# Optimization experiments

Hardware: AMD Instinct MI355X
Metric: run time of the kernel (lower is better)

## Reference

```python
import jax, jax.numpy as jnp
import numpy as np

N, E = 100000, 1600000
H, F, G = 128, 128, 51   # hidden_channels, num_filters, num_gaussians
CUTOFF = 10.0
LOG2 = 0.6931471805599453

def ssp(x):
    # ShiftedSoftplus: softplus(x) - log(2)
    return jax.nn.softplus(x) - jnp.asarray(LOG2, x.dtype)

def setup_inputs() -> dict:
    key = jax.random.key(0)
    ks = jax.random.split(key, 16)
    s = 0.05
    return {
        "z": jax.random.normal(ks[0], (N, H), dtype=jnp.float32),
        "pos": jax.random.uniform(ks[1], (N, 3), dtype=jnp.float32),
        "edge_index": jax.random.randint(ks[2], (2, E), 0, N, dtype=jnp.int64),
        # CFConv linears
        "lin1_w": jax.random.normal(ks[3], (F, H), dtype=jnp.float32) * s,   # no bias
        "lin2_w": jax.random.normal(ks[4], (H, F), dtype=jnp.float32) * s,
        "lin2_b": jnp.zeros((H,), dtype=jnp.float32),
        # edge-filter MLP: Linear(G,F) -> ssp -> Linear(F,F)
        "mlp0_w": jax.random.normal(ks[5], (F, G), dtype=jnp.float32) * s,
        "mlp0_b": jnp.zeros((F,), dtype=jnp.float32),
        "mlp2_w": jax.random.normal(ks[6], (F, F), dtype=jnp.float32) * s,
        "mlp2_b": jnp.zeros((F,), dtype=jnp.float32),
        # InteractionBlock output linear
        "blk_w": jax.random.normal(ks[7], (H, H), dtype=jnp.float32) * s,
        "blk_b": jnp.zeros((H,), dtype=jnp.float32),
        # SchNetLayer head: lin1 -> ssp -> lin2
        "out1_w": jax.random.normal(ks[8], (H, H), dtype=jnp.float32) * s,
        "out1_b": jnp.zeros((H,), dtype=jnp.float32),
        "out2_w": jax.random.normal(ks[9], (H, H), dtype=jnp.float32) * s,
        "out2_b": jnp.zeros((H,), dtype=jnp.float32),
    }

def reference(z, pos, edge_index, lin1_w, lin2_w, lin2_b, mlp0_w, mlp0_b,
              mlp2_w, mlp2_b, blk_w, blk_b, out1_w, out1_b, out2_w, out2_b):
    row, col = edge_index[0], edge_index[1]
    # edge distances
    d = pos[row] - pos[col]                          # [E,3]
    ew = jnp.sqrt(jnp.sum(d * d, axis=-1) + 1e-12)   # [E]
    # GaussianSmearing(0, cutoff, G)
    offset = jnp.linspace(0.0, CUTOFF, G).astype(ew.dtype)
    coeff = -0.5 / (CUTOFF / (G - 1)) ** 2
    ea = jnp.exp(coeff * (ew[:, None] - offset[None, :]) ** 2)  # [E,G]
    # cosine cutoff envelope
    C = 0.5 * (jnp.cos(ew * (jnp.pi / CUTOFF)) + 1.0)           # [E]
    # edge-conditioned filter W = mlp(edge_attr) * C
    W = ssp(ea @ mlp0_w.T + mlp0_b) @ mlp2_w.T + mlp2_b         # [E,F]
    W = W * C[:, None]
    # CFConv: lin1 -> gather(x_j) * W -> scatter-add -> lin2
    x1 = z @ lin1_w.T                                            # [N,F]
    msg = x1[row] * W                                            # [E,F]
    agg = jax.ops.segment_sum(msg, col, num_segments=z.shape[0]) # [N,F]
    conv = agg @ lin2_w.T + lin2_b                               # [N,H]
    # InteractionBlock: act -> lin, residual add
    h = z + (ssp(conv) @ blk_w.T + blk_b)
    # head: lin1 -> ssp -> lin2
    h = ssp(h @ out1_w.T + out1_b) @ out2_w.T + out2_b
    return h
```

## Files before the change

kernel.cpp:

```cpp
#include <hip/hip_runtime.h>
#include <math.h>


#define HDIM 128
#define GDIM 51
#define TAB_T 2048
#define TAB_PTS (TAB_T + 1)
#define RMAX 1.7330f
#define INV_STEP ((float)TAB_T / RMAX)
#define WMAT 2048
#define SCB 2048

typedef short short8 __attribute__((ext_vector_type(8)));
typedef float floatx4 __attribute__((ext_vector_type(4)));

__device__ __forceinline__ float ssp_f(float x) {
  float t = __expf(-fabsf(x));
  return fmaxf(x, 0.0f) + __logf(1.0f + t) - 0.6931471805599453f;
}
__device__ __forceinline__ float bl(unsigned int u) { return __uint_as_float(u << 16); }
__device__ __forceinline__ float bh(unsigned int u) { return __uint_as_float(u & 0xFFFF0000u); }
__device__ __forceinline__ unsigned short f2bf(float f) {
  unsigned int u = __float_as_uint(f);
  unsigned int r = u + 0x7FFFu + ((u >> 16) & 1u);
  return (unsigned short)(r >> 16);
}
__device__ __forceinline__ unsigned int pack_bf16(float a, float b) {
  unsigned int r;
  asm("v_cvt_pk_bf16_f32 %0, %1, %2" : "=v"(r) : "v"(a), "v"(b));
  return r;
}

__global__ void prep_kernel(const float* __restrict__ lin1, const float* __restrict__ lin2,
                            const float* __restrict__ blkw, const float* __restrict__ o1w,
                            const float* __restrict__ o2w, const float* __restrict__ m0w,
                            const float* __restrict__ m2w,
                            unsigned short* __restrict__ wbf,
                            float* __restrict__ m0t, float* __restrict__ m2t) {
  int gid = blockIdx.x * blockDim.x + threadIdx.x;
  int stride = gridDim.x * blockDim.x;
  for (int idx = gid; idx < 5 * 16384; idx += stride) {
    int mat = idx >> 14;
    int o   = idx & 16383;
    int idx4 = o >> 3;
    int jj   = o & 7;
    int ct   = idx4 >> 8;
    int kk   = (idx4 >> 6) & 3;
    int lane = idx4 & 63;
    int c = ct * 16 + (lane & 15);
    int g = kk * 4 + (lane >> 4);
    const float* w = (mat == 0) ? lin1 : (mat == 1) ? lin2 : (mat == 2) ? blkw
                   : (mat == 3) ? o1w : o2w;
    wbf[idx] = f2bf(w[c * HDIM + g * 8 + jj]);
  }
  for (int idx = gid; idx < GDIM * HDIM; idx += stride) {
    int g = idx >> 7, f = idx & 127;
    m0t[idx] = m0w[f * GDIM + g];
  }
  for (int idx = gid; idx < HDIM * HDIM; idx += stride) {
    int j = idx >> 7, f = idx & 127;
    m2t[idx] = m2w[f * HDIM + j];
  }
}

__global__ __launch_bounds__(128) void table_kernel(
    const float* __restrict__ m0t, const float* __restrict__ m0b,
    const float* __restrict__ m2t, const float* __restrict__ m2b,
    unsigned int* __restrict__ tabb) {
  __shared__ float ea[GDIM];
  __shared__ float h1[HDIM];
  int f = threadIdx.x;
  float b0 = m0b[f];
  float b2 = m2b[f];
  for (int t = blockIdx.x; t < TAB_PTS; t += gridDim.x) {
    float ew = (float)t * (RMAX / (float)TAB_T);
    if (f < GDIM) {
      float dd = ew - (float)f * 0.2f;
      ea[f] = expf(-12.5f * dd * dd);
    }
    __syncthreads();
    float s = b0;
    #pragma unroll 3
    for (int g = 0; g < GDIM; ++g) s = fmaf(ea[g], m0t[g * HDIM + f], s);
    h1[f] = ssp_f(s);
    __syncthreads();
    float s2 = b2;
    #pragma unroll 4
    for (int j = 0; j < HDIM; ++j) s2 = fmaf(h1[j], m2t[j * HDIM + f], s2);
    float C = 0.5f * (cosf(ew * 0.31415926535897931f) + 1.0f);
    float val = s2 * C;
    float pr = __shfl_xor(val, 1);
    if ((f & 1) == 0) tabb[(size_t)t * 64 + (f >> 1)] = pack_bf16(val, pr);
    __syncthreads();
  }
}

__device__ __forceinline__ short8 frag_ld(const unsigned int* __restrict__ slab,
                                          int row, int g) {
  const uint4 v = *(const uint4*)(slab + row * 64 + (((g << 2) ^ ((row & 7) << 2))));
  return __builtin_bit_cast(short8, v);
}

__device__ __forceinline__ void stage_act64(unsigned int* __restrict__ slab,
                                            const float* __restrict__ src,
                                            int n0, int N, int t) {
  #pragma unroll
  for (int i = 0; i < 8; ++i) {
    int id = t + i * 256;
    int r  = id >> 5;
    int k4 = id & 31;
    int gn = n0 + r;
    float4 v = make_float4(0.f, 0.f, 0.f, 0.f);
    if (gn < N) v = *(const float4*)(src + (size_t)gn * HDIM + k4 * 4);
    int w = (k4 * 2) ^ ((r & 7) * 4);
    *(uint2*)(slab + r * 64 + w) = make_uint2(pack_bf16(v.x, v.y), pack_bf16(v.z, v.w));
  }
}

__device__ __forceinline__ void stage_mm8(const unsigned int* __restrict__ Aslab,
                                          const uint4* __restrict__ wm,
                                          floatx4 acc[8], int wave, int lane) {
  int m = lane & 15, q = lane >> 4;
  int r0 = wave * 16 + m;
  #pragma unroll
  for (int ct = 0; ct < 8; ++ct) acc[ct] = (floatx4){0.f, 0.f, 0.f, 0.f};
  #pragma unroll
  for (int kk = 0; kk < 4; ++kk) {
    short8 a = frag_ld(Aslab, r0, kk * 4 + q);
    #pragma unroll
    for (int ct = 0; ct < 8; ++ct) {
      short8 b = __builtin_bit_cast(short8, wm[(ct * 4 + kk) * 64 + lane]);
      acc[ct] = __builtin_amdgcn_mfma_f32_16x16x32_bf16(a, b, acc[ct], 0, 0, 0);
    }
  }
}

__device__ __forceinline__ void mm_cs1(const unsigned int* __restrict__ Aslab,
                                       const uint4* __restrict__ wm,
                                       floatx4 acc[4], int ct, int lane) {
  int m = lane & 15, q = lane >> 4;
  #pragma unroll
  for (int mr = 0; mr < 4; ++mr) acc[mr] = (floatx4){0.f, 0.f, 0.f, 0.f};
  #pragma unroll
  for (int kk = 0; kk < 4; ++kk) {
    short8 b = __builtin_bit_cast(short8, wm[(ct * 4 + kk) * 64 + lane]);
    #pragma unroll
    for (int mr = 0; mr < 4; ++mr) {
      short8 a = frag_ld(Aslab, mr * 16 + m, kk * 4 + q);
      acc[mr] = __builtin_amdgcn_mfma_f32_16x16x32_bf16(a, b, acc[mr], 0, 0, 0);
    }
  }
}

__device__ __forceinline__ void wb_cs1(unsigned int* __restrict__ slab,
                                       const floatx4 acc[4], float bias,
                                       int ct, int lane, bool do_ssp) {
  int m = lane & 15, q = lane >> 4;
  bool act = ((m ^ ct) & 1) == 0;
  int k2 = ct * 8 + (m >> 1);
  #pragma unroll
  for (int mr = 0; mr < 4; ++mr) {
    #pragma unroll
    for (int r = 0; r < 4; ++r) {
      float v = acc[mr][r] + bias;
      if (do_ssp) v = ssp_f(v);
      float pr = __shfl_xor(v, 1);
      if (act) {
        int R = mr * 16 + q * 4 + r;
        slab[R * 64 + (k2 ^ ((R & 7) * 4))] = (m & 1) ? pack_bf16(pr, v)
                                                      : pack_bf16(v, pr);
      }
    }
  }
}

__global__ __launch_bounds__(256) void x1_kernel(const float* __restrict__ z,
    const uint4* __restrict__ wbf4, unsigned int* __restrict__ x1b, int N) {
  __shared__ unsigned int Aslab[64 * 64];
  int t = threadIdx.x, wave = t >> 6, lane = t & 63;
  int m = lane & 15, q = lane >> 4;
  int n0 = blockIdx.x * 64;
  stage_act64(Aslab, z, n0, N, t);
  __syncthreads();
  floatx4 acc[8];
  stage_mm8(Aslab, wbf4, acc, wave, lane);
  #pragma unroll
  for (int ct = 0; ct < 8; ++ct) {
    #pragma unroll
    for (int r = 0; r < 4; ++r) {
      float v = acc[ct][r];
      float pr = __shfl_xor(v, 1);
      int gr = n0 + wave * 16 + q * 4 + r;
      if (((m ^ ct) & 1) == 0 && gr < N)
        x1b[(size_t)gr * 64 + ct * 8 + (m >> 1)] = (m & 1) ? pack_bf16(pr, v)
                                                           : pack_bf16(v, pr);
    }
  }
}

__global__ __launch_bounds__(256) void hist_kernel(const int* __restrict__ ei,
                                                   int* __restrict__ count, int E) {
  int gid = blockIdx.x * blockDim.x + threadIdx.x;
  int stride = gridDim.x * blockDim.x;
  for (int e = gid; e < E; e += stride)
    atomicAdd(&count[ei[E + e]], 1);
}

__global__ __launch_bounds__(256) void scan1_kernel(const int* __restrict__ count,
                                                    int* __restrict__ bsum, int N) {
  int b = blockIdx.x, t = threadIdx.x;
  int base = b * SCB;
  int s = 0;
  for (int i = t; i < SCB; i += 256) {
    int gi = base + i;
    s += (gi < N) ? count[gi] : 0;
  }
  #pragma unroll
  for (int d = 32; d >= 1; d >>= 1) s += __shfl_down(s, d);
  __shared__ int ws[4];
  if ((t & 63) == 0) ws[t >> 6] = s;
  __syncthreads();
  if (t == 0) bsum[b] = ws[0] + ws[1] + ws[2] + ws[3];
}

__global__ __launch_bounds__(64) void scan2_kernel(const int* __restrict__ bsum,
    int* __restrict__ boff, int* __restrict__ startN, int NB) {
  int lane = threadIdx.x;
  int carry = 0;
  for (int base = 0; base < NB; base += 64) {
    int i = base + lane;
    int v = (i < NB) ? bsum[i] : 0;
    int x = v;
    #pragma unroll
    for (int d = 1; d < 64; d <<= 1) {
      int y = __shfl_up(x, d);
      if (lane >= d) x += y;
    }
    if (i < NB) boff[i] = carry + x - v;
    carry += __shfl(x, 63);
  }
  if (lane == 0) *startN = carry;
}

__global__ __launch_bounds__(256) void scan3_kernel(const int* __restrict__ count,
    const int* __restrict__ boff, int* __restrict__ start, int* __restrict__ cursor,
    int N) {
  int b = blockIdx.x, t = threadIdx.x;
  int lane = t & 63, w = t >> 6;
  int loc = b * SCB + t * 8;
  int v[8];
  int s = 0;
  #pragma unroll
  for (int j = 0; j < 8; ++j) {
    int gi = loc + j;
    v[j] = (gi < N) ? count[gi] : 0;
    s += v[j];
  }
  int x = s;
  #pragma unroll
  for (int d = 1; d < 64; d <<= 1) {
    int y = __shfl_up(x, d);
    if (lane >= d) x += y;
  }
  __shared__ int ws[4];
  if (lane == 63) ws[w] = x;
  __syncthreads();
  int wbase = 0;
  #pragma unroll
  for (int k = 0; k < 3; ++k) wbase += (k < w) ? ws[k] : 0;
  int excl = boff[b] + wbase + x - s;
  #pragma unroll
  for (int j = 0; j < 8; ++j) {
    int gi = loc + j;
    if (gi < N) { start[gi] = excl; cursor[gi] = excl; }
    excl += v[j];
  }
}

__global__ __launch_bounds__(256) void scatter_kernel(const int* __restrict__ ei,
    const float* __restrict__ pos, int* __restrict__ cursor,
    unsigned int* __restrict__ srec, int E) {
  int gid = blockIdx.x * blockDim.x + threadIdx.x;
  int stride = gridDim.x * blockDim.x;
  for (int e = gid; e < E; e += stride) {
    int row = ei[e];
    int col = ei[E + e];
    float dx = pos[row * 3]     - pos[col * 3];
    float dy = pos[row * 3 + 1] - pos[col * 3 + 1];
    float dz = pos[row * 3 + 2] - pos[col * 3 + 2];
    float ew = sqrtf(dx * dx + dy * dy + dz * dz + 1e-12f);
    float u = ew * INV_STEP;
    int t0 = min((int)u, TAB_T - 1);
    float fr = u - (float)t0;
    int f4 = min((int)(fr * 16.0f), 15);
    unsigned int rec = ((unsigned int)row << 15) | ((unsigned int)t0 << 4)
                     | (unsigned int)f4;
    int p = atomicAdd(&cursor[col], 1);
    srec[p] = rec;
  }
}

__device__ __forceinline__ void edge_acc(unsigned int rec,
                                         const unsigned int* __restrict__ x1b,
                                         const unsigned int* __restrict__ tabb,
                                         int lane, float& ax, float& ay) {
  int row = (int)(rec >> 15);
  int t0  = (int)((rec >> 4) & 2047u);
  float fr = (float)(rec & 15u) * 0.0625f + 0.03125f;
  unsigned int xw = x1b[(size_t)row * 64 + lane];
  unsigned int w0 = tabb[(size_t)t0 * 64 + lane];
  unsigned int w1 = tabb[(size_t)t0 * 64 + 64 + lane];
  float wa = fmaf(fr, bl(w1) - bl(w0), bl(w0));
  float wb = fmaf(fr, bh(w1) - bh(w0), bh(w0));
  ax = fmaf(bl(xw), wa, ax);
  ay = fmaf(bh(xw), wb, ay);
}

__global__ __launch_bounds__(256) void agg_kernel(const unsigned int* __restrict__ srec,
    const int* __restrict__ start, const unsigned int* __restrict__ x1b,
    const unsigned int* __restrict__ tabb, unsigned int* __restrict__ aggb, int N) {
  int wid = (int)((blockIdx.x * 256 + threadIdx.x) >> 6);
  int lane = threadIdx.x & 63;
  if (wid >= N) return;
  int s = start[wid], e = start[wid + 1];
  float ax = 0.f, ay = 0.f;
  int i = s;
  for (; i + 8 <= e; i += 8) {
    unsigned int r[8];
    #pragma unroll
    for (int j = 0; j < 8; ++j) r[j] = srec[i + j];
    #pragma unroll
    for (int j = 0; j < 8; ++j) edge_acc(r[j], x1b, tabb, lane, ax, ay);
  }
  if (i + 4 <= e) {
    unsigned int r[4];
    #pragma unroll
    for (int j = 0; j < 4; ++j) r[j] = srec[i + j];
    #pragma unroll
    for (int j = 0; j < 4; ++j) edge_acc(r[j], x1b, tabb, lane, ax, ay);
    i += 4;
  }
  for (; i < e; ++i) edge_acc(srec[i], x1b, tabb, lane, ax, ay);
  aggb[(size_t)wid * 64 + lane] = pack_bf16(ax, ay);
}

__global__ __launch_bounds__(512) void epilogue_kernel(
    const unsigned int* __restrict__ aggb, const float* __restrict__ z,
    const uint4* __restrict__ wbf4,
    const float* __restrict__ b_lin2, const float* __restrict__ b_blk,
    const float* __restrict__ b_o1, const float* __restrict__ b_o2,
    float* __restrict__ out, int N) {
  __shared__ unsigned int Aslab[2][64 * 64];
  int t = threadIdx.x, wave = t >> 6, lane = t & 63;
  int m = lane & 15, q = lane >> 4;
  int n0 = blockIdx.x * 64;
  int ct = wave;
  bool act = ((m ^ ct) & 1) == 0;
  int k2 = ct * 8 + (m >> 1);
  int cb = ct * 16 + (m & ~1);
  floatx4 acc[4];

  float bs1 = b_lin2[ct * 16 + m];
  float bs2 = b_blk [ct * 16 + m];
  float bs3 = b_o1  [ct * 16 + m];
  float bs4 = b_o2  [ct * 16 + m];

  #pragma unroll
  for (int i = 0; i < 4; ++i) {
    int id = t + i * 512;
    int r  = id >> 5;
    int k22 = id & 31;
    int gn = n0 + r;
    uint2 v = make_uint2(0u, 0u);
    if (gn < N) v = *(const uint2*)(aggb + (size_t)gn * 64 + k22 * 2);
    *(uint2*)(Aslab[0] + r * 64 + ((k22 * 2) ^ ((r & 7) * 4))) = v;
  }
  __syncthreads();

  mm_cs1(Aslab[0], wbf4 + 1 * WMAT, acc, ct, lane);
  wb_cs1(Aslab[1], acc, bs1, ct, lane, true);
  __syncthreads();

  mm_cs1(Aslab[1], wbf4 + 2 * WMAT, acc, ct, lane);
  #pragma unroll
  for (int mr = 0; mr < 4; ++mr) {
    #pragma unroll
    for (int r = 0; r < 4; ++r) {
      int gr = n0 + mr * 16 + q * 4 + r;
      float2 zz = make_float2(0.f, 0.f);
      if (act && gr < N) zz = *(const float2*)(z + (size_t)gr * HDIM + cb);
      float mine  = (m & 1) ? zz.y : zz.x;
      float yours = (m & 1) ? zz.x : zz.y;
      float other = __shfl_xor(yours, 1);
      float zval = act ? mine : other;
      float v = acc[mr][r] + bs2 + zval;
      float pr = __shfl_xor(v, 1);
      if (act) {
        int R = mr * 16 + q * 4 + r;
        Aslab[0][R * 64 + (k2 ^ ((R & 7) * 4))] = (m & 1) ? pack_bf16(pr, v)
                                                          : pack_bf16(v, pr);
      }
    }
  }
  __syncthreads();

  mm_cs1(Aslab[0], wbf4 + 3 * WMAT, acc, ct, lane);
  wb_cs1(Aslab[1], acc, bs3, ct, lane, true);
  __syncthreads();

  mm_cs1(Aslab[1], wbf4 + 4 * WMAT, acc, ct, lane);
  #pragma unroll
  for (int mr = 0; mr < 4; ++mr) {
    #pragma unroll
    for (int r = 0; r < 4; ++r) {
      float v = acc[mr][r] + bs4;
      float pr = __shfl_xor(v, 1);
      int gr = n0 + mr * 16 + q * 4 + r;
      if (act && gr < N) {
        float lo = (m & 1) ? pr : v;
        float hi = (m & 1) ? v : pr;
        *(float2*)(out + (size_t)gr * HDIM + cb) = make_float2(lo, hi);
      }
    }
  }
}

extern "C" void kernel_launch(void* const* d_in, const int* in_sizes, int n_in,
                              void* d_out, int out_size, void* d_ws, size_t ws_size,
                              hipStream_t stream) {
  const float* z     = (const float*)d_in[0];
  const float* pos   = (const float*)d_in[1];
  const int*   ei    = (const int*)d_in[2];
  const float* lin1  = (const float*)d_in[3];
  const float* lin2  = (const float*)d_in[4];
  const float* blin2 = (const float*)d_in[5];
  const float* m0w   = (const float*)d_in[6];
  const float* m0b   = (const float*)d_in[7];
  const float* m2w   = (const float*)d_in[8];
  const float* m2b   = (const float*)d_in[9];
  const float* blkw  = (const float*)d_in[10];
  const float* blkb  = (const float*)d_in[11];
  const float* o1w   = (const float*)d_in[12];
  const float* o1b   = (const float*)d_in[13];
  const float* o2w   = (const float*)d_in[14];
  const float* o2b   = (const float*)d_in[15];
  float* out = (float*)d_out;
  const int N = in_sizes[0] / HDIM;
  const int E = in_sizes[2] / 2;
  const int NB = (N + SCB - 1) / SCB;

  char* wsb = (char*)d_ws;
  size_t off = 0;
  auto alloc = [&](size_t bytes) {
    void* p = wsb + off;
    off += (bytes + 15) & ~(size_t)15;
    return p;
  };
  unsigned int* x1b  = (unsigned int*)alloc((size_t)N * 64 * 4);
  unsigned int* aggb = (unsigned int*)alloc((size_t)N * 64 * 4);
  unsigned int* tabb = (unsigned int*)alloc((size_t)TAB_PTS * 64 * 4);
  float* m0t  = (float*)alloc((size_t)GDIM * HDIM * 4);
  float* m2t  = (float*)alloc((size_t)HDIM * HDIM * 4);
  unsigned short* wbf = (unsigned short*)alloc(5 * 16384 * 2);
  int* count  = (int*)alloc(((size_t)N + 1) * 4);
  int* start  = (int*)alloc(((size_t)N + 1) * 4);
  int* cursor = (int*)alloc(((size_t)N + 1) * 4);
  int* bsum   = (int*)alloc(((size_t)NB + 1) * 4);
  int* boff   = (int*)alloc(((size_t)NB + 1) * 4);
  unsigned int* srec = (unsigned int*)alloc((size_t)E * 4);

  const int ngrid = (N + 63) / 64;
  prep_kernel<<<256, 256, 0, stream>>>(lin1, lin2, blkw, o1w, o2w, m0w, m2w,
                                       wbf, m0t, m2t);
  hipMemsetAsync(count, 0, ((size_t)N + 1) * 4, stream);
  hist_kernel<<<2048, 256, 0, stream>>>(ei, count, E);
  scan1_kernel<<<NB, 256, 0, stream>>>(count, bsum, N);
  scan2_kernel<<<1, 64, 0, stream>>>(bsum, boff, start + N, NB);
  scan3_kernel<<<NB, 256, 0, stream>>>(count, boff, start, cursor, N);
  scatter_kernel<<<2048, 256, 0, stream>>>(ei, pos, cursor, srec, E);
  table_kernel<<<512, 128, 0, stream>>>(m0t, m0b, m2t, m2b, tabb);
  x1_kernel<<<ngrid, 256, 0, stream>>>(z, (const uint4*)wbf, x1b, N);
  agg_kernel<<<(N + 3) / 4, 256, 0, stream>>>(srec, start, x1b, tabb, aggb, N);
  epilogue_kernel<<<ngrid, 512, 0, stream>>>(aggb, z, (const uint4*)wbf, blin2,
                                             blkb, o1b, o2b, out, N);
}
```

Baseline: 470.2 us.

## Fuse histogram with edge record computation and replace atomic scatter by rank-based permutation

New measurement: 421.3 us. 10.4% less time.

```diff
diff --git a/kernel.cpp b/kernel.cpp
--- a/kernel.cpp
+++ b/kernel.cpp
@@ -198,88 +198,9 @@
   }
 }
 
-__global__ __launch_bounds__(256) void hist_kernel(const int* __restrict__ ei,
-                                                   int* __restrict__ count, int E) {
-  int gid = blockIdx.x * blockDim.x + threadIdx.x;
-  int stride = gridDim.x * blockDim.x;
-  for (int e = gid; e < E; e += stride)
-    atomicAdd(&count[ei[E + e]], 1);
-}
-
-__global__ __launch_bounds__(256) void scan1_kernel(const int* __restrict__ count,
-                                                    int* __restrict__ bsum, int N) {
-  int b = blockIdx.x, t = threadIdx.x;
-  int base = b * SCB;
-  int s = 0;
-  for (int i = t; i < SCB; i += 256) {
-    int gi = base + i;
-    s += (gi < N) ? count[gi] : 0;
-  }
-  #pragma unroll
-  for (int d = 32; d >= 1; d >>= 1) s += __shfl_down(s, d);
-  __shared__ int ws[4];
-  if ((t & 63) == 0) ws[t >> 6] = s;
-  __syncthreads();
-  if (t == 0) bsum[b] = ws[0] + ws[1] + ws[2] + ws[3];
-}
-
-__global__ __launch_bounds__(64) void scan2_kernel(const int* __restrict__ bsum,
-    int* __restrict__ boff, int* __restrict__ startN, int NB) {
-  int lane = threadIdx.x;
-  int carry = 0;
-  for (int base = 0; base < NB; base += 64) {
-    int i = base + lane;
-    int v = (i < NB) ? bsum[i] : 0;
-    int x = v;
-    #pragma unroll
-    for (int d = 1; d < 64; d <<= 1) {
-      int y = __shfl_up(x, d);
-      if (lane >= d) x += y;
-    }
-    if (i < NB) boff[i] = carry + x - v;
-    carry += __shfl(x, 63);
-  }
-  if (lane == 0) *startN = carry;
-}
-
-__global__ __launch_bounds__(256) void scan3_kernel(const int* __restrict__ count,
-    const int* __restrict__ boff, int* __restrict__ start, int* __restrict__ cursor,
-    int N) {
-  int b = blockIdx.x, t = threadIdx.x;
-  int lane = t & 63, w = t >> 6;
-  int loc = b * SCB + t * 8;
-  int v[8];
-  int s = 0;
-  #pragma unroll
-  for (int j = 0; j < 8; ++j) {
-    int gi = loc + j;
-    v[j] = (gi < N) ? count[gi] : 0;
-    s += v[j];
-  }
-  int x = s;
-  #pragma unroll
-  for (int d = 1; d < 64; d <<= 1) {
-    int y = __shfl_up(x, d);
-    if (lane >= d) x += y;
-  }
-  __shared__ int ws[4];
-  if (lane == 63) ws[w] = x;
-  __syncthreads();
-  int wbase = 0;
-  #pragma unroll
-  for (int k = 0; k < 3; ++k) wbase += (k < w) ? ws[k] : 0;
-  int excl = boff[b] + wbase + x - s;
-  #pragma unroll
-  for (int j = 0; j < 8; ++j) {
-    int gi = loc + j;
-    if (gi < N) { start[gi] = excl; cursor[gi] = excl; }
-    excl += v[j];
-  }
-}
-
-__global__ __launch_bounds__(256) void scatter_kernel(const int* __restrict__ ei,
-    const float* __restrict__ pos, int* __restrict__ cursor,
-    unsigned int* __restrict__ srec, int E) {
+__global__ __launch_bounds__(256) void edge_kernel(const int* __restrict__ ei,
+    const float* __restrict__ pos, int* __restrict__ count,
+    unsigned int* __restrict__ erec, int* __restrict__ erank, int E) {
   int gid = blockIdx.x * blockDim.x + threadIdx.x;
   int stride = gridDim.x * blockDim.x;
   for (int e = gid; e < E; e += stride) {
@@ -293,10 +214,90 @@
     int t0 = min((int)u, TAB_T - 1);
     float fr = u - (float)t0;
     int f4 = min((int)(fr * 16.0f), 15);
-    unsigned int rec = ((unsigned int)row << 15) | ((unsigned int)t0 << 4)
-                     | (unsigned int)f4;
-    int p = atomicAdd(&cursor[col], 1);
-    srec[p] = rec;
+    erec[e] = ((unsigned int)row << 15) | ((unsigned int)t0 << 4)
+            | (unsigned int)f4;
+    erank[e] = atomicAdd(&count[col], 1);
+  }
+}
+
+__global__ __launch_bounds__(256) void scan1_kernel(const int* __restrict__ count,
+                                                    int* __restrict__ bsum, int N) {
+  int b = blockIdx.x, t = threadIdx.x;
+  int base = b * SCB;
+  int s = 0;
+  for (int i = t; i < SCB; i += 256) {
+    int gi = base + i;
+    s += (gi < N) ? count[gi] : 0;
+  }
+  #pragma unroll
+  for (int d = 32; d >= 1; d >>= 1) s += __shfl_down(s, d);
+  __shared__ int ws[4];
+  if ((t & 63) == 0) ws[t >> 6] = s;
+  __syncthreads();
+  if (t == 0) bsum[b] = ws[0] + ws[1] + ws[2] + ws[3];
+}
+
+__global__ __launch_bounds__(64) void scan2_kernel(const int* __restrict__ bsum,
+    int* __restrict__ boff, int* __restrict__ startN, int NB) {
+  int lane = threadIdx.x;
+  int carry = 0;
+  for (int base = 0; base < NB; base += 64) {
+    int i = base + lane;
+    int v = (i < NB) ? bsum[i] : 0;
+    int x = v;
+    #pragma unroll
+    for (int d = 1; d < 64; d <<= 1) {
+      int y = __shfl_up(x, d);
+      if (lane >= d) x += y;
+    }
+    if (i < NB) boff[i] = carry + x - v;
+    carry += __shfl(x, 63);
+  }
+  if (lane == 0) *startN = carry;
+}
+
+__global__ __launch_bounds__(256) void scan3_kernel(const int* __restrict__ count,
+    const int* __restrict__ boff, int* __restrict__ start, int N) {
+  int b = blockIdx.x, t = threadIdx.x;
+  int lane = t & 63, w = t >> 6;
+  int loc = b * SCB + t * 8;
+  int v[8];
+  int s = 0;
+  #pragma unroll
+  for (int j = 0; j < 8; ++j) {
+    int gi = loc + j;
+    v[j] = (gi < N) ? count[gi] : 0;
+    s += v[j];
+  }
+  int x = s;
+  #pragma unroll
+  for (int d = 1; d < 64; d <<= 1) {
+    int y = __shfl_up(x, d);
+    if (lane >= d) x += y;
+  }
+  __shared__ int ws[4];
+  if (lane == 63) ws[w] = x;
+  __syncthreads();
+  int wbase = 0;
+  #pragma unroll
+  for (int k = 0; k < 3; ++k) wbase += (k < w) ? ws[k] : 0;
+  int excl = boff[b] + wbase + x - s;
+  #pragma unroll
+  for (int j = 0; j < 8; ++j) {
+    int gi = loc + j;
+    if (gi < N) start[gi] = excl;
+    excl += v[j];
+  }
+}
+
+__global__ __launch_bounds__(256) void perm_kernel(const int* __restrict__ ei,
+    const unsigned int* __restrict__ erec, const int* __restrict__ erank,
+    const int* __restrict__ start, unsigned int* __restrict__ srec, int E) {
+  int gid = blockIdx.x * blockDim.x + threadIdx.x;
+  int stride = gridDim.x * blockDim.x;
+  for (int e = gid; e < E; e += stride) {
+    int col = ei[E + e];
+    srec[start[col] + erank[e]] = erec[e];
   }
 }
 
@@ -464,20 +465,21 @@
   unsigned short* wbf = (unsigned short*)alloc(5 * 16384 * 2);
   int* count  = (int*)alloc(((size_t)N + 1) * 4);
   int* start  = (int*)alloc(((size_t)N + 1) * 4);
-  int* cursor = (int*)alloc(((size_t)N + 1) * 4);
   int* bsum   = (int*)alloc(((size_t)NB + 1) * 4);
   int* boff   = (int*)alloc(((size_t)NB + 1) * 4);
-  unsigned int* srec = (unsigned int*)alloc((size_t)E * 4);
+  unsigned int* srec  = (unsigned int*)alloc((size_t)E * 4);
+  unsigned int* erec  = (unsigned int*)alloc((size_t)E * 4);
+  int*          erank = (int*)alloc((size_t)E * 4);
 
   const int ngrid = (N + 63) / 64;
   prep_kernel<<<256, 256, 0, stream>>>(lin1, lin2, blkw, o1w, o2w, m0w, m2w,
                                        wbf, m0t, m2t);
   hipMemsetAsync(count, 0, ((size_t)N + 1) * 4, stream);
-  hist_kernel<<<2048, 256, 0, stream>>>(ei, count, E);
+  edge_kernel<<<2048, 256, 0, stream>>>(ei, pos, count, erec, erank, E);
   scan1_kernel<<<NB, 256, 0, stream>>>(count, bsum, N);
   scan2_kernel<<<1, 64, 0, stream>>>(bsum, boff, start + N, NB);
-  scan3_kernel<<<NB, 256, 0, stream>>>(count, boff, start, cursor, N);
-  scatter_kernel<<<2048, 256, 0, stream>>>(ei, pos, cursor, srec, E);
+  scan3_kernel<<<NB, 256, 0, stream>>>(count, boff, start, N);
+  perm_kernel<<<2048, 256, 0, stream>>>(ei, erec, erank, start, srec, E);
   table_kernel<<<512, 128, 0, stream>>>(m0t, m0b, m2t, m2b, tabb);
   x1_kernel<<<ngrid, 256, 0, stream>>>(z, (const uint4*)wbf, x1b, N);
   agg_kernel<<<(N + 3) / 4, 256, 0, stream>>>(srec, start, x1b, tabb, aggb, N);
```
